# Kernel tuning notes

Measured on AMD Instinct MI355X. Metric: run time of the kernel, lower is better.

Reference implementation:

```python
import jax, jax.numpy as jnp
import numpy as np

B, C, E = 4, 2048, 1024
H = 16
HD = E // H  # 64

def setup_inputs() -> dict:
    key = jax.random.key(0)
    k1, k2, k3 = jax.random.split(key, 3)
    x = jax.random.normal(k1, (B, C, E), dtype=jnp.float32)
    W_attn = jax.random.normal(k2, (E, 3 * E), dtype=jnp.float32) * 0.02
    W_proj = jax.random.normal(k3, (E, E), dtype=jnp.float32) * 0.02
    return {"x": x, "W_attn": W_attn, "W_proj": W_proj}

def reference(x, W_attn, W_proj):
    b, c, e = x.shape
    qkv = x @ W_attn                      # [B,C,3E]
    q, k, v = jnp.split(qkv, 3, axis=-1)
    # [B,C,E] -> [B,H,C,HD]
    q = q.reshape(b, c, H, HD).transpose(0, 2, 1, 3)
    k = k.reshape(b, c, H, HD).transpose(0, 2, 1, 3)
    v = v.reshape(b, c, H, HD).transpose(0, 2, 1, 3)
    scale = 1.0 / np.sqrt(HD).astype(np.float32)
    att = jnp.einsum('bhqd,bhkd->bhqk', q, k) * scale  # [B,H,C,C]
    causal = jnp.tril(jnp.ones((c, c), dtype=bool))
    att = jnp.where(causal[None, None, :, :], att, -jnp.inf)
    att = jax.nn.softmax(att, axis=-1)
    y = jnp.einsum('bhqk,bhkd->bhqd', att, v)          # [B,H,C,HD]
    y = y.transpose(0, 2, 1, 3).reshape(b, c, e)
    return y @ W_proj
```

## Files before the change

kernel.cpp:

```cpp
#include <hip/hip_runtime.h>
#include <hip/hip_bf16.h>


typedef unsigned short ushort_t;
typedef __attribute__((ext_vector_type(8))) short short8;
typedef __attribute__((ext_vector_type(4))) float floatx4;
typedef __attribute__((ext_vector_type(16))) float floatx16;
typedef __attribute__((ext_vector_type(2))) unsigned uintx2;

#define NH   16
#define SEQ  2048
#define EMB  1024
#define HDIM 64

#define MFMA32(a, b, c) __builtin_amdgcn_mfma_f32_32x32x16_bf16(a, b, c, 0, 0, 0)
#define MFMA16(a, b, c) __builtin_amdgcn_mfma_f32_16x16x32_bf16(a, b, c, 0, 0, 0)
#define WAITVM4() asm volatile("s_waitcnt vmcnt(4)" ::: "memory")
#define WAITVM0() asm volatile("s_waitcnt vmcnt(0)" ::: "memory")

__device__ __forceinline__ ushort_t f2bf(float f) {
    union { float f; unsigned u; } v; v.f = f;
    unsigned r = (v.u + 0x7fffu + ((v.u >> 16) & 1u)) >> 16;
    return (ushort_t)r;
}

__device__ __forceinline__ unsigned cvtpk(float lo, float hi) {
    unsigned r;
    asm("v_cvt_pk_bf16_f32 %0, %1, %2" : "=v"(r) : "v"(lo), "v"(hi));
    return r;
}

__device__ __forceinline__ uintx2 pl32(unsigned a, unsigned b) {
    return __builtin_amdgcn_permlane32_swap(a, b, false, false);
}

__device__ __forceinline__ short8 mk8(unsigned a, unsigned b, unsigned c, unsigned d) {
    union { unsigned w[4]; short8 s; } t;
    t.w[0] = a; t.w[1] = b; t.w[2] = c; t.w[3] = d;
    return t.s;
}

#if defined(__has_builtin) && __has_builtin(__builtin_amdgcn_global_load_lds)
#define HAS_GLL 1
__device__ __forceinline__ void gload16(const ushort_t* g, ushort_t* l) {
    __builtin_amdgcn_global_load_lds((const __attribute__((address_space(1))) void*)g,
                                     (__attribute__((address_space(3))) void*)l, 16, 0, 0);
}
#else
#define HAS_GLL 0
#endif

__global__ __launch_bounds__(256) void cast_k(const float* __restrict__ in,
                                              ushort_t* __restrict__ out) {
    int i = blockIdx.x * 256 + threadIdx.x;
    float4 v0 = ((const float4*)in)[i * 2];
    float4 v1 = ((const float4*)in)[i * 2 + 1];
    short8 t;
    t[0] = (short)f2bf(v0.x); t[1] = (short)f2bf(v0.y);
    t[2] = (short)f2bf(v0.z); t[3] = (short)f2bf(v0.w);
    t[4] = (short)f2bf(v1.x); t[5] = (short)f2bf(v1.y);
    t[6] = (short)f2bf(v1.z); t[7] = (short)f2bf(v1.w);
    ((short8*)out)[i] = t;
}

__global__ void transpose_cast_k(const float* __restrict__ in, ushort_t* __restrict__ out,
                                 int R, int Cc, float sc, int ncut) {
    __shared__ ushort_t tile[32][33];
    int x  = blockIdx.x * 32 + threadIdx.x;
    int y0 = blockIdx.y * 32;
    float s = (x < ncut) ? sc : 1.0f;
#pragma unroll
    for (int i = 0; i < 32; i += 8)
        tile[threadIdx.y + i][threadIdx.x] = f2bf(in[(size_t)(y0 + threadIdx.y + i) * Cc + x] * s);
    __syncthreads();
    int xo = blockIdx.y * 32 + threadIdx.x;
    int yo = blockIdx.x * 32;
#pragma unroll
    for (int i = 0; i < 32; i += 8)
        out[(size_t)(yo + threadIdx.y + i) * R + xo] = tile[threadIdx.x][threadIdx.y + i];
}

template<int EPI>
__global__ __launch_bounds__(256) void gemm_bt(const ushort_t* __restrict__ A,
                                               const ushort_t* __restrict__ Bt,
                                               void* __restrict__ O0v,
                                               ushort_t* __restrict__ O1,
                                               ushort_t* __restrict__ O2,
                                               int M, int N, int K) {
    __shared__ __align__(16) ushort_t As[128 * 64];
    __shared__ __align__(16) ushort_t Bs[128 * 64];
    const int tid  = threadIdx.x;
    const int wv   = tid >> 6, lane = tid & 63, quad = lane >> 4, l15 = lane & 15;
    const int wm   = wv >> 1, wn = wv & 1;
    const int bm   = blockIdx.x, bn = blockIdx.y;
    const int lrow = lane >> 3;
    const int kg   = (lane & 7) ^ (lrow & 7);
    const int sw   = l15 & 7;

    floatx4 acc[4][4];
#pragma unroll
    for (int i = 0; i < 4; i++)
#pragma unroll
        for (int j = 0; j < 4; j++) acc[i][j] = (floatx4){0.f, 0.f, 0.f, 0.f};

    for (int kt = 0; kt < K; kt += 64) {
#pragma unroll
        for (int it = 0; it < 4; it++) {
            int r0 = it * 32 + wv * 8;
            const ushort_t* ga = &A [(size_t)(bm * 128 + r0 + lrow) * K + kt + kg * 8];
            const ushort_t* gb = &Bt[(size_t)(bn * 128 + r0 + lrow) * K + kt + kg * 8];
#if HAS_GLL
            gload16(ga, &As[r0 * 64]);
            gload16(gb, &Bs[r0 * 64]);
#else
            *(uint4*)&As[(r0 + lrow) * 64 + (lane & 7) * 8] = *(const uint4*)ga;
            *(uint4*)&Bs[(r0 + lrow) * 64 + (lane & 7) * 8] = *(const uint4*)gb;
#endif
        }
        __syncthreads();
#pragma unroll
        for (int ks = 0; ks < 2; ks++) {
            short8 af[4], bf[4];
#pragma unroll
            for (int i = 0; i < 4; i++)
                af[i] = *(const short8*)&As[(wm * 64 + i * 16 + l15) * 64 + (((ks * 4 + quad) ^ sw) * 8)];
#pragma unroll
            for (int j = 0; j < 4; j++)
                bf[j] = *(const short8*)&Bs[(wn * 64 + j * 16 + l15) * 64 + (((ks * 4 + quad) ^ sw) * 8)];
#pragma unroll
            for (int i = 0; i < 4; i++)
#pragma unroll
                for (int j = 0; j < 4; j++)
                    acc[i][j] = MFMA16(af[i], bf[j], acc[i][j]);
        }
        __syncthreads();
    }

    if (EPI == 0) {
#pragma unroll
        for (int i = 0; i < 4; i++)
#pragma unroll
            for (int j = 0; j < 4; j++)
#pragma unroll
                for (int r = 0; r < 4; r++) {
                    int row = bm * 128 + wm * 64 + i * 16 + quad * 4 + r;
                    int col = bn * 128 + wn * 64 + j * 16 + l15;
                    ((float*)O0v)[(size_t)row * N + col] = acc[i][j][r];
                }
    } else {
#pragma unroll
        for (int i = 0; i < 4; i++)
#pragma unroll
            for (int j = 0; j < 4; j++) {
                int row0 = bm * 128 + wm * 64 + i * 16 + quad * 4;
                int col  = bn * 128 + wn * 64 + j * 16 + l15;
                int b = row0 >> 11;
                int which = col >> 10, nn = col & 1023;
                int hh = nn >> 6, d = nn & 63;
                if (which == 2) {
                    uint2 pv;
                    pv.x = cvtpk(acc[i][j][0], acc[i][j][1]);
                    pv.y = cvtpk(acc[i][j][2], acc[i][j][3]);
                    *(uint2*)&O2[((size_t)(b * NH + hh) * HDIM + d) * SEQ + (row0 & 2047)] = pv;
                } else {
                    ushort_t* dst = (which == 0) ? (ushort_t*)O0v : O1;
#pragma unroll
                    for (int r = 0; r < 4; r++)
                        dst[((size_t)(b * NH + hh) * SEQ + ((row0 + r) & 2047)) * HDIM + d] =
                            f2bf(acc[i][j][r]);
                }
            }
    }
}

__device__ __forceinline__ void stage_kv(const ushort_t* __restrict__ Kg,
                                         const ushort_t* __restrict__ Vtg,
                                         ushort_t* Kn, ushort_t* Vn,
                                         int bh, int j, int wv, int lane) {
    const int lrow = lane >> 3;
    const int kgs  = (lane & 7) ^ (lrow & 7);
#pragma unroll
    for (int it = 0; it < 2; it++) {
        int r0 = it * 32 + wv * 8;
        const ushort_t* gk = &Kg [((size_t)bh * SEQ  + j * 64 + r0 + lrow) * HDIM + kgs * 8];
        const ushort_t* gv = &Vtg[((size_t)bh * HDIM + r0 + lrow) * SEQ + j * 64 + kgs * 8];
#if HAS_GLL
        gload16(gk, &Kn[r0 * 64]);
        gload16(gv, &Vn[r0 * 64]);
#else
        *(uint4*)&Kn[(r0 + lrow) * 64 + (lane & 7) * 8] = *(const uint4*)gk;
        *(uint4*)&Vn[(r0 + lrow) * 64 + (lane & 7) * 8] = *(const uint4*)gv;
#endif
    }
}

__global__ __launch_bounds__(256) void attn3_k(const ushort_t* __restrict__ Qg,
                                               const ushort_t* __restrict__ Kg,
                                               const ushort_t* __restrict__ Vtg,
                                               ushort_t* __restrict__ Y) {
    __shared__ __align__(16) ushort_t SM[3 * 8192];
    const int tid  = threadIdx.x;
    const int wv   = tid >> 6, lane = tid & 63;
    const int l31  = lane & 31, hf = lane >> 5;
    const int bh   = blockIdx.x, z = blockIdx.y;
    const int qb   = 15 - z;
    const int qs7  = l31 & 7;
    const int b = bh >> 4, hh = bh & 15;

    const int qrow0 = qb * 128 + wv * 32;
    const int q_abs = qrow0 + l31;
    const int jmax_w = 2 * qb + (wv >> 1);
    const int nj = 2 * qb + 2;

    short8 qf[4];
    {
        const ushort_t* qp = Qg + ((size_t)bh * SEQ + q_abs) * HDIM + hf * 8;
#pragma unroll
        for (int ks = 0; ks < 4; ks++) qf[ks] = *(const short8*)(qp + ks * 16);
    }

    floatx16 o0, o1;
#pragma unroll
    for (int r = 0; r < 16; r++) { o0[r] = 0.f; o1[r] = 0.f; }
    float l_i = 0.f;

    stage_kv(Kg, Vtg, SM,        SM + 4096,  bh, 0, wv, lane);
    stage_kv(Kg, Vtg, SM + 8192, SM + 12288, bh, 1, wv, lane);
    WAITVM4();
    __builtin_amdgcn_s_barrier();

    int cur = 0, stg = 2;
    for (int j = 0; j < nj; j++) {
        ushort_t* Ks = SM + cur * 8192;
        ushort_t* Vs = Ks + 4096;

        const bool issue = (j + 2 < nj);
        if (issue) {
            ushort_t* Kn = SM + stg * 8192;
            stage_kv(Kg, Vtg, Kn, Kn + 4096, bh, j + 2, wv, lane);
        }

        if (j <= jmax_w) {
            floatx16 s0, s1;
#pragma unroll
            for (int r = 0; r < 16; r++) { s0[r] = 0.f; s1[r] = 0.f; }
            __builtin_amdgcn_s_setprio(1);
#pragma unroll
            for (int ks = 0; ks < 4; ks++) {
                int slot = ((hf + 2 * ks) ^ qs7) * 8;
                short8 k0 = *(const short8*)&Ks[l31 * 64 + slot];
                short8 k1 = *(const short8*)&Ks[(32 + l31) * 64 + slot];
                s0 = MFMA32(k0, qf[ks], s0);
                s1 = MFMA32(k1, qf[ks], s1);
            }
            __builtin_amdgcn_s_setprio(0);

            if (j == jmax_w) {
                const int kb0 = j * 64 + 4 * hf;
#pragma unroll
                for (int r = 0; r < 16; r++) {
                    int key = kb0 + (r & 3) + 8 * (r >> 2);
                    if (key > q_abs)      s0[r] = -1e30f;
                    if (key + 32 > q_abs) s1[r] = -1e30f;
                }
            }

            float rs0 = 0.f, rs1 = 0.f;
#pragma unroll
            for (int r = 0; r < 16; r++) {
                s0[r] = __builtin_amdgcn_exp2f(s0[r]);
                s1[r] = __builtin_amdgcn_exp2f(s1[r]);
                rs0 += s0[r]; rs1 += s1[r];
            }
            float rs = rs0 + rs1;
            rs += __shfl_xor(rs, 32);
            l_i += rs;

            unsigned u0[8], u1[8];
#pragma unroll
            for (int g = 0; g < 4; g++) {
                u0[2 * g]     = cvtpk(s0[g * 4],     s0[g * 4 + 1]);
                u0[2 * g + 1] = cvtpk(s0[g * 4 + 2], s0[g * 4 + 3]);
                u1[2 * g]     = cvtpk(s1[g * 4],     s1[g * 4 + 1]);
                u1[2 * g + 1] = cvtpk(s1[g * 4 + 2], s1[g * 4 + 3]);
            }
            unsigned pw[16];
#pragma unroll
            for (int tt = 0; tt < 2; tt++) {
                const unsigned* u = tt ? u1 : u0;
#pragma unroll
                for (int p = 0; p < 2; p++) {
#pragma unroll
                    for (int i = 0; i < 2; i++) {
                        uintx2 r = pl32(u[4 * p + i], u[4 * p + 2 + i]);
                        pw[8 * tt + 4 * p + i]     = r[0];
                        pw[8 * tt + 4 * p + 2 + i] = r[1];
                    }
                }
            }

            __builtin_amdgcn_s_setprio(1);
#pragma unroll
            for (int ks = 0; ks < 4; ks++) {
                int slot = ((hf + 2 * ks) ^ qs7) * 8;
                short8 v0 = *(const short8*)&Vs[l31 * 64 + slot];
                short8 v1 = *(const short8*)&Vs[(32 + l31) * 64 + slot];
                short8 pf = mk8(pw[4 * ks], pw[4 * ks + 1], pw[4 * ks + 2], pw[4 * ks + 3]);
                o0 = MFMA32(v0, pf, o0);
                o1 = MFMA32(v1, pf, o1);
            }
            __builtin_amdgcn_s_setprio(0);
        }

        if (issue) { WAITVM4(); } else { WAITVM0(); }
        __builtin_amdgcn_s_barrier();
        cur = (cur == 2) ? 0 : cur + 1;
        stg = (stg == 2) ? 0 : stg + 1;
    }

    ushort_t* Ew = SM + wv * 2048;
    float inv = 1.0f / l_i;
#pragma unroll
    for (int g = 0; g < 4; g++) {
        uint2 w0, w1;
        w0.x = cvtpk(o0[g * 4] * inv,     o0[g * 4 + 1] * inv);
        w0.y = cvtpk(o0[g * 4 + 2] * inv, o0[g * 4 + 3] * inv);
        w1.x = cvtpk(o1[g * 4] * inv,     o1[g * 4 + 1] * inv);
        w1.y = cvtpk(o1[g * 4 + 2] * inv, o1[g * 4 + 3] * inv);
        *(uint2*)&Ew[l31 * 64 + ((g       ^ qs7) * 8) + 4 * hf] = w0;
        *(uint2*)&Ew[l31 * 64 + (((4 + g) ^ qs7) * 8) + 4 * hf] = w1;
    }
    const int dg = lane & 7;
#pragma unroll
    for (int sb = 0; sb < 4; sb++) {
        int ql = sb * 8 + (lane >> 3);
        uint4 v = *(const uint4*)&Ew[ql * 64 + ((dg ^ (ql & 7)) * 8)];
        *(uint4*)&Y[((size_t)(b * SEQ + qrow0 + ql)) * EMB + hh * HDIM + dg * 8] = v;
    }
}

extern "C" void kernel_launch(void* const* d_in, const int* in_sizes, int n_in,
                              void* d_out, int out_size, void* d_ws, size_t ws_size,
                              hipStream_t stream) {
    const float* x      = (const float*)d_in[0];
    const float* W_attn = (const float*)d_in[1];
    const float* W_proj = (const float*)d_in[2];

    char* ws = (char*)d_ws;
    ushort_t* Wt_attn = (ushort_t*)(ws);
    ushort_t* Wt_proj = (ushort_t*)(ws + 6291456);
    ushort_t* Xb      = (ushort_t*)(ws + 8388608);
    ushort_t* Yb      = Xb;
    ushort_t* Qb      = (ushort_t*)(ws + 25165824);
    ushort_t* Kb      = (ushort_t*)(ws + 41943040);
    ushort_t* Vt      = (ushort_t*)(ws + 58720256);

    const float c2 = 0.18033688011112042f;

    cast_k<<<4096, 256, 0, stream>>>(x, Xb);
    transpose_cast_k<<<dim3(3072 / 32, 1024 / 32), dim3(32, 8), 0, stream>>>(W_attn, Wt_attn,
                                                                             1024, 3072, c2, 1024);
    transpose_cast_k<<<dim3(1024 / 32, 1024 / 32), dim3(32, 8), 0, stream>>>(W_proj, Wt_proj,
                                                                             1024, 1024, 1.0f, 0);
    gemm_bt<1><<<dim3(8192 / 128, 3072 / 128), 256, 0, stream>>>(Xb, Wt_attn, Qb, Kb, Vt,
                                                                 8192, 3072, 1024);
    attn3_k<<<dim3(64, 16), 256, 0, stream>>>(Qb, Kb, Vt, Yb);
    gemm_bt<0><<<dim3(8192 / 128, 1024 / 128), 256, 0, stream>>>(Yb, Wt_proj, (float*)d_out,
                                                                 nullptr, nullptr, 8192, 1024, 1024);
}
```

Baseline: 239.4 us.

## Double-buffer GEMM LDS staging and split projection GEMM into 64-row tiles

```diff
diff --git a/kernel.cpp b/kernel.cpp
--- a/kernel.cpp
+++ b/kernel.cpp
@@ -48,6 +48,10 @@
 }
 #else
 #define HAS_GLL 0
+__device__ __forceinline__ void gload16(const ushort_t* g, ushort_t* l) {
+    int lane = threadIdx.x & 63;
+    *(uint4*)(l + lane * 8) = *(const uint4*)g;
+}
 #endif
 
 __global__ __launch_bounds__(256) void cast_k(const float* __restrict__ in,
@@ -80,21 +84,18 @@
         out[(size_t)(yo + threadIdx.y + i) * R + xo] = tile[threadIdx.x][threadIdx.y + i];
 }
 
-template<int EPI>
-__global__ __launch_bounds__(256) void gemm_bt(const ushort_t* __restrict__ A,
-                                               const ushort_t* __restrict__ Bt,
-                                               void* __restrict__ O0v,
-                                               ushort_t* __restrict__ O1,
-                                               ushort_t* __restrict__ O2,
-                                               int M, int N, int K) {
-    __shared__ __align__(16) ushort_t As[128 * 64];
-    __shared__ __align__(16) ushort_t Bs[128 * 64];
+__global__ __launch_bounds__(256) void gemm_qkv(const ushort_t* __restrict__ A,
+                                                const ushort_t* __restrict__ Bt,
+                                                ushort_t* __restrict__ Qo,
+                                                ushort_t* __restrict__ Ko,
+                                                ushort_t* __restrict__ Vto) {
+    __shared__ __align__(16) ushort_t SM[2 * 16384];
     const int tid  = threadIdx.x;
     const int wv   = tid >> 6, lane = tid & 63, quad = lane >> 4, l15 = lane & 15;
     const int wm   = wv >> 1, wn = wv & 1;
     const int bm   = blockIdx.x, bn = blockIdx.y;
     const int lrow = lane >> 3;
-    const int kg   = (lane & 7) ^ (lrow & 7);
+    const int kg   = (lane & 7) ^ lrow;
     const int sw   = l15 & 7;
 
     floatx4 acc[4][4];
@@ -103,21 +104,25 @@
 #pragma unroll
         for (int j = 0; j < 4; j++) acc[i][j] = (floatx4){0.f, 0.f, 0.f, 0.f};
 
-    for (int kt = 0; kt < K; kt += 64) {
+    auto stage = [&](int buf, int kt) {
+        ushort_t* Ab = &SM[buf * 16384];
+        ushort_t* Bb = Ab + 8192;
 #pragma unroll
         for (int it = 0; it < 4; it++) {
             int r0 = it * 32 + wv * 8;
-            const ushort_t* ga = &A [(size_t)(bm * 128 + r0 + lrow) * K + kt + kg * 8];
-            const ushort_t* gb = &Bt[(size_t)(bn * 128 + r0 + lrow) * K + kt + kg * 8];
-#if HAS_GLL
-            gload16(ga, &As[r0 * 64]);
-            gload16(gb, &Bs[r0 * 64]);
-#else
-            *(uint4*)&As[(r0 + lrow) * 64 + (lane & 7) * 8] = *(const uint4*)ga;
-            *(uint4*)&Bs[(r0 + lrow) * 64 + (lane & 7) * 8] = *(const uint4*)gb;
-#endif
-        }
-        __syncthreads();
+            gload16(&A [(size_t)(bm * 128 + r0 + lrow) * 1024 + kt + kg * 8], &Ab[r0 * 64]);
+            gload16(&Bt[(size_t)(bn * 128 + r0 + lrow) * 1024 + kt + kg * 8], &Bb[r0 * 64]);
+        }
+    };
+
+    stage(0, 0);
+    WAITVM0();
+    __builtin_amdgcn_s_barrier();
+
+    for (int t = 0; t < 16; t++) {
+        if (t < 15) stage((t + 1) & 1, (t + 1) * 64);
+        const ushort_t* As = &SM[(t & 1) * 16384];
+        const ushort_t* Bs = As + 8192;
 #pragma unroll
         for (int ks = 0; ks < 2; ks++) {
             short8 af[4], bf[4];
@@ -127,50 +132,113 @@
 #pragma unroll
             for (int j = 0; j < 4; j++)
                 bf[j] = *(const short8*)&Bs[(wn * 64 + j * 16 + l15) * 64 + (((ks * 4 + quad) ^ sw) * 8)];
+            __builtin_amdgcn_s_setprio(1);
 #pragma unroll
             for (int i = 0; i < 4; i++)
 #pragma unroll
                 for (int j = 0; j < 4; j++)
                     acc[i][j] = MFMA16(af[i], bf[j], acc[i][j]);
-        }
-        __syncthreads();
-    }
-
-    if (EPI == 0) {
-#pragma unroll
-        for (int i = 0; i < 4; i++)
-#pragma unroll
-            for (int j = 0; j < 4; j++)
-#pragma unroll
-                for (int r = 0; r < 4; r++) {
-                    int row = bm * 128 + wm * 64 + i * 16 + quad * 4 + r;
-                    int col = bn * 128 + wn * 64 + j * 16 + l15;
-                    ((float*)O0v)[(size_t)row * N + col] = acc[i][j][r];
-                }
-    } else {
-#pragma unroll
-        for (int i = 0; i < 4; i++)
-#pragma unroll
-            for (int j = 0; j < 4; j++) {
-                int row0 = bm * 128 + wm * 64 + i * 16 + quad * 4;
-                int col  = bn * 128 + wn * 64 + j * 16 + l15;
-                int b = row0 >> 11;
-                int which = col >> 10, nn = col & 1023;
-                int hh = nn >> 6, d = nn & 63;
-                if (which == 2) {
-                    uint2 pv;
-                    pv.x = cvtpk(acc[i][j][0], acc[i][j][1]);
-                    pv.y = cvtpk(acc[i][j][2], acc[i][j][3]);
-                    *(uint2*)&O2[((size_t)(b * NH + hh) * HDIM + d) * SEQ + (row0 & 2047)] = pv;
-                } else {
-                    ushort_t* dst = (which == 0) ? (ushort_t*)O0v : O1;
-#pragma unroll
-                    for (int r = 0; r < 4; r++)
-                        dst[((size_t)(b * NH + hh) * SEQ + ((row0 + r) & 2047)) * HDIM + d] =
-                            f2bf(acc[i][j][r]);
-                }
-            }
-    }
+            __builtin_amdgcn_s_setprio(0);
+        }
+        if (t < 15) { WAITVM0(); }
+        __builtin_amdgcn_s_barrier();
+    }
+
+#pragma unroll
+    for (int i = 0; i < 4; i++)
+#pragma unroll
+        for (int j = 0; j < 4; j++) {
+            int row0 = bm * 128 + wm * 64 + i * 16 + quad * 4;
+            int col  = bn * 128 + wn * 64 + j * 16 + l15;
+            int b = row0 >> 11;
+            int which = col >> 10, nn = col & 1023;
+            int hh = nn >> 6, d = nn & 63;
+            if (which == 2) {
+                uint2 pv;
+                pv.x = cvtpk(acc[i][j][0], acc[i][j][1]);
+                pv.y = cvtpk(acc[i][j][2], acc[i][j][3]);
+                *(uint2*)&Vto[((size_t)(b * NH + hh) * HDIM + d) * SEQ + (row0 & 2047)] = pv;
+            } else {
+                ushort_t* dst = (which == 0) ? Qo : Ko;
+#pragma unroll
+                for (int r = 0; r < 4; r++)
+                    dst[((size_t)(b * NH + hh) * SEQ + ((row0 + r) & 2047)) * HDIM + d] =
+                        f2bf(acc[i][j][r]);
+            }
+        }
+}
+
+__global__ __launch_bounds__(256) void gemm_proj(const ushort_t* __restrict__ A,
+                                                 const ushort_t* __restrict__ Bt,
+                                                 float* __restrict__ O) {
+    __shared__ __align__(16) ushort_t SM[2 * 12288];
+    const int tid  = threadIdx.x;
+    const int wv   = tid >> 6, lane = tid & 63, quad = lane >> 4, l15 = lane & 15;
+    const int bm   = blockIdx.x, bn = blockIdx.y;
+    const int lrow = lane >> 3;
+    const int kg   = (lane & 7) ^ lrow;
+    const int sw   = l15 & 7;
+
+    floatx4 acc[4][2];
+#pragma unroll
+    for (int i = 0; i < 4; i++)
+#pragma unroll
+        for (int j = 0; j < 2; j++) acc[i][j] = (floatx4){0.f, 0.f, 0.f, 0.f};
+
+    auto stage = [&](int buf, int kt) {
+        ushort_t* Ab = &SM[buf * 12288];
+        ushort_t* Bb = Ab + 4096;
+#pragma unroll
+        for (int it = 0; it < 2; it++) {
+            int r0 = it * 32 + wv * 8;
+            gload16(&A[(size_t)(bm * 64 + r0 + lrow) * 1024 + kt + kg * 8], &Ab[r0 * 64]);
+        }
+#pragma unroll
+        for (int it = 0; it < 4; it++) {
+            int r0 = it * 32 + wv * 8;
+            gload16(&Bt[(size_t)(bn * 128 + r0 + lrow) * 1024 + kt + kg * 8], &Bb[r0 * 64]);
+        }
+    };
+
+    stage(0, 0);
+    WAITVM0();
+    __builtin_amdgcn_s_barrier();
+
+    for (int t = 0; t < 16; t++) {
+        if (t < 15) stage((t + 1) & 1, (t + 1) * 64);
+        const ushort_t* As = &SM[(t & 1) * 12288];
+        const ushort_t* Bs = As + 4096;
+#pragma unroll
+        for (int ks = 0; ks < 2; ks++) {
+            short8 af[4], bf[2];
+#pragma unroll
+            for (int i = 0; i < 4; i++)
+                af[i] = *(const short8*)&As[(i * 16 + l15) * 64 + (((ks * 4 + quad) ^ sw) * 8)];
+#pragma unroll
+            for (int j = 0; j < 2; j++)
+                bf[j] = *(const short8*)&Bs[(wv * 32 + j * 16 + l15) * 64 + (((ks * 4 + quad) ^ sw) * 8)];
+            __builtin_amdgcn_s_setprio(1);
+#pragma unroll
+            for (int i = 0; i < 4; i++)
+#pragma unroll
+                for (int j = 0; j < 2; j++)
+                    acc[i][j] = MFMA16(af[i], bf[j], acc[i][j]);
+            __builtin_amdgcn_s_setprio(0);
+        }
+        if (t < 15) { WAITVM0(); }
+        __builtin_amdgcn_s_barrier();
+    }
+
+#pragma unroll
+    for (int i = 0; i < 4; i++)
+#pragma unroll
+        for (int j = 0; j < 2; j++)
+#pragma unroll
+            for (int r = 0; r < 4; r++) {
+                int row = bm * 64 + i * 16 + quad * 4 + r;
+                int col = bn * 128 + wv * 32 + j * 16 + l15;
+                O[(size_t)row * 1024 + col] = acc[i][j][r];
+            }
 }
 
 __device__ __forceinline__ void stage_kv(const ushort_t* __restrict__ Kg,
@@ -184,13 +252,8 @@
         int r0 = it * 32 + wv * 8;
         const ushort_t* gk = &Kg [((size_t)bh * SEQ  + j * 64 + r0 + lrow) * HDIM + kgs * 8];
         const ushort_t* gv = &Vtg[((size_t)bh * HDIM + r0 + lrow) * SEQ + j * 64 + kgs * 8];
-#if HAS_GLL
         gload16(gk, &Kn[r0 * 64]);
         gload16(gv, &Vn[r0 * 64]);
-#else
-        *(uint4*)&Kn[(r0 + lrow) * 64 + (lane & 7) * 8] = *(const uint4*)gk;
-        *(uint4*)&Vn[(r0 + lrow) * 64 + (lane & 7) * 8] = *(const uint4*)gv;
-#endif
     }
 }
 
@@ -362,9 +425,7 @@
                                                                              1024, 3072, c2, 1024);
     transpose_cast_k<<<dim3(1024 / 32, 1024 / 32), dim3(32, 8), 0, stream>>>(W_proj, Wt_proj,
                                                                              1024, 1024, 1.0f, 0);
-    gemm_bt<1><<<dim3(8192 / 128, 3072 / 128), 256, 0, stream>>>(Xb, Wt_attn, Qb, Kb, Vt,
-                                                                 8192, 3072, 1024);
+    gemm_qkv<<<dim3(64, 24), 256, 0, stream>>>(Xb, Wt_attn, Qb, Kb, Vt);
     attn3_k<<<dim3(64, 16), 256, 0, stream>>>(Qb, Kb, Vt, Yb);
-    gemm_bt<0><<<dim3(8192 / 128, 1024 / 128), 256, 0, stream>>>(Yb, Wt_proj, (float*)d_out,
-                                                                 nullptr, nullptr, 8192, 1024, 1024);
-}
+    gemm_proj<<<dim3(128, 8), 256, 0, stream>>>(Yb, Wt_proj, (float*)d_out);
+}
```

Result: no change. 241.3 us (+0.8%).
